# Optimization experiments

Hardware: AMD Instinct MI355X
Metric: run time of the kernel (lower is better)

The kernel has to match this reference:

```python
import jax, jax.numpy as jnp
import numpy as np

N = 8192
IN_F = 256
OUT_F = 64
ALPHA = 0.2
NEG_INF = -9e15


def setup_inputs() -> dict:
    key = jax.random.key(0)
    k1, k2, k3, k4 = jax.random.split(key, 4)
    h = jax.random.normal(k1, (N, IN_F), dtype=jnp.float32)
    W = jax.random.normal(k2, (IN_F, OUT_F), dtype=jnp.float32) * (1.414 / np.sqrt(IN_F))
    a = jax.random.normal(k3, (2 * OUT_F, 1), dtype=jnp.float32) * (1.414 / np.sqrt(2 * OUT_F))
    adj = jax.random.randint(k4, (N, N), 0, 2, dtype=jnp.int32)
    return {"h": h, "W": W, "a": a, "adj": adj}


def reference(h, W, a, adj):
    # Wh: [N, F]
    Wh = h @ W
    # Decompose concat-based attention: e_ij = LeakyReLU(Wh_i . a[:F] + Wh_j . a[F:])
    a1, a2 = a[:OUT_F], a[OUT_F:]
    src = Wh @ a1              # [N, 1] contribution of row i
    dst = Wh @ a2              # [N, 1] contribution of col j
    e = jax.nn.leaky_relu(src + dst.T, negative_slope=ALPHA)  # [N, N]
    e = jnp.where(adj > 0, e, NEG_INF)
    attention = jax.nn.softmax(e, axis=1)
    # dropout is identity in eval mode
    h_prime = attention @ Wh   # [N, F]
    return h_prime
```

## Files before the change

### kernel.cpp

```cpp
#include <hip/hip_runtime.h>

#define NROWS 8192
#define NSPLIT 8
#define JT (NROWS / NSPLIT)
#define NITER (JT / 64)
#define L2E 1.4426950408889634f

typedef __attribute__((ext_vector_type(4))) float f32x4;
typedef __attribute__((ext_vector_type(8))) __bf16 bf16x8;
typedef __attribute__((ext_vector_type(4))) unsigned int u32x4;

__device__ __forceinline__ unsigned short f2bf(float x) {
  unsigned u = __float_as_uint(x);
  u += 0x7fffu + ((u >> 16) & 1u);
  return (unsigned short)(u >> 16);
}

__global__ __launch_bounds__(256) void k_prep(
    const float* __restrict__ h, const float* __restrict__ W,
    const float* __restrict__ a, unsigned short* __restrict__ WhB,
    float* __restrict__ src, float* __restrict__ dst) {
  int i = blockIdx.x * 4 + (threadIdx.x >> 6);
  int lane = threadIdx.x & 63;
  const float* hrow = h + (size_t)i * 256;
  float s = 0.f;
#pragma unroll 4
  for (int k = 0; k < 256; k += 4) {
    float4 hv = *(const float4*)(hrow + k);
    s = fmaf(hv.x, W[(k + 0) * 64 + lane], s);
    s = fmaf(hv.y, W[(k + 1) * 64 + lane], s);
    s = fmaf(hv.z, W[(k + 2) * 64 + lane], s);
    s = fmaf(hv.w, W[(k + 3) * 64 + lane], s);
  }
  int nt = lane >> 4, c = lane & 15;
  int gi = (i >> 3) & 3, e = i & 7;
  int idx = ((((i >> 5) * 4 + nt) * 64) + c + 16 * gi) * 8 + e;
  WhB[idx] = f2bf(s);
  float v1 = s * a[lane];
  float v2 = s * a[64 + lane];
#pragma unroll
  for (int d = 32; d; d >>= 1) {
    v1 += __shfl_xor(v1, d);
    v2 += __shfl_xor(v2, d);
  }
  if (lane == 0) {
    src[i] = v1 * L2E;
    dst[i] = v2 * L2E;
  }
}

__global__ __launch_bounds__(256) void k_dmax(
    const float* __restrict__ dst, float* __restrict__ dmax) {
  __shared__ float red[4];
  float v = -INFINITY;
  for (int i = threadIdx.x; i < NROWS; i += 256) v = fmaxf(v, dst[i]);
#pragma unroll
  for (int d = 32; d; d >>= 1) v = fmaxf(v, __shfl_xor(v, d));
  if ((threadIdx.x & 63) == 0) red[threadIdx.x >> 6] = v;
  __syncthreads();
  if (threadIdx.x == 0)
    *dmax = fmaxf(fmaxf(red[0], red[1]), fmaxf(red[2], red[3]));
}

__global__ __launch_bounds__(256, 4) void k_attn(
    const int* __restrict__ adj, const unsigned short* __restrict__ WhB,
    const float* __restrict__ src, const float* __restrict__ dst,
    const float* __restrict__ dmax,
    float* __restrict__ pl, float* __restrict__ pacc) {
  __shared__ float ldst[JT];
  int task = blockIdx.x * 4 + (threadIdx.x >> 6);
  int sp = task >> 9;
  int mt = task & 511;
  int lane = threadIdx.x & 63;
  int r = lane & 15;
  int g = lane >> 4;
  int row0 = mt * 16;
  int jbase = sp * JT;

  for (int k = threadIdx.x; k < JT; k += 256) ldst[k] = dst[jbase + k];
  __syncthreads();

  unsigned long long mk0 = 0, mk1 = 0, mk2 = 0, mk3 = 0;
  {
    const int* abase = adj + (size_t)row0 * NROWS + jbase + lane;
#pragma unroll
    for (int rr = 0; rr < 16; ++rr) {
      const int* rp = abase + (size_t)rr * NROWS;
#pragma unroll
      for (int ch = 0; ch < 16; ++ch) {
        int v = rp[ch * 64];
        unsigned long long bal = __ballot(v > 0);
        const int holder = ((ch & 3) << 4) + rr;
        if ((ch >> 2) == 0) mk0 = (lane == holder) ? bal : mk0;
        if ((ch >> 2) == 1) mk1 = (lane == holder) ? bal : mk1;
        if ((ch >> 2) == 2) mk2 = (lane == holder) ? bal : mk2;
        if ((ch >> 2) == 3) mk3 = (lane == holder) ? bal : mk3;
      }
    }
  }

  float srcr = src[row0 + r];
  float vB = srcr + *dmax;
  float Mi = fmaxf(vB, 0.2f * vB);

  float lrow = 0.f;
  f32x4 acc[4] = {f32x4{0.f, 0.f, 0.f, 0.f}, f32x4{0.f, 0.f, 0.f, 0.f},
                  f32x4{0.f, 0.f, 0.f, 0.f}, f32x4{0.f, 0.f, 0.f, 0.f}};
  const bf16x8* Bfr = (const bf16x8*)WhB;

#pragma unroll
  for (int it = 0; it < NITER; ++it) {
    const int jb = it * 64;

    unsigned long long pw;
    if ((it >> 2) == 0) pw = __shfl(mk0, ((it & 3) << 4) + r);
    if ((it >> 2) == 1) pw = __shfl(mk1, ((it & 3) << 4) + r);
    if ((it >> 2) == 2) pw = __shfl(mk2, ((it & 3) << 4) + r);
    if ((it >> 2) == 3) pw = __shfl(mk3, ((it & 3) << 4) + r);

    int jc = (jbase + jb) >> 5;
    const bf16x8* bp = Bfr + (size_t)jc * 256 + lane;
    bf16x8 b0 = bp[0];
    bf16x8 b1 = bp[64];
    bf16x8 b2 = bp[128];
    bf16x8 b3 = bp[192];
    bf16x8 b4 = bp[256];
    bf16x8 b5 = bp[320];
    bf16x8 b6 = bp[384];
    bf16x8 b7 = bp[448];

    const float* dl = ldst + jb + 8 * g;
    float4 d0 = *(const float4*)(dl);
    float4 d1 = *(const float4*)(dl + 4);
    float4 d2 = *(const float4*)(dl + 32);
    float4 d3 = *(const float4*)(dl + 36);

    unsigned lo = (unsigned)(pw >> (8 * g));
    unsigned hi = (unsigned)(pw >> (32 + 8 * g));

    float p[16];
#define PE(P, BIT, DD)                    \
  {                                       \
    float v_ = srcr + (DD);               \
    v_ = fmaxf(v_, 0.2f * v_);            \
    float e_ = exp2f(v_ - Mi);            \
    (P) = (BIT) ? e_ : 0.f;               \
  }
    PE(p[0], lo & 1u, d0.x)   PE(p[1], lo & 2u, d0.y)
    PE(p[2], lo & 4u, d0.z)   PE(p[3], lo & 8u, d0.w)
    PE(p[4], lo & 16u, d1.x)  PE(p[5], lo & 32u, d1.y)
    PE(p[6], lo & 64u, d1.z)  PE(p[7], lo & 128u, d1.w)
    PE(p[8], hi & 1u, d2.x)   PE(p[9], hi & 2u, d2.y)
    PE(p[10], hi & 4u, d2.z)  PE(p[11], hi & 8u, d2.w)
    PE(p[12], hi & 16u, d3.x) PE(p[13], hi & 32u, d3.y)
    PE(p[14], hi & 64u, d3.z) PE(p[15], hi & 128u, d3.w)
#undef PE

    unsigned q[8];
#pragma unroll
    for (int t = 0; t < 16; t += 2) {
      lrow += p[t] + p[t + 1];
      unsigned qq;
      asm("v_cvt_pk_bf16_f32 %0, %1, %2" : "=v"(qq) : "v"(p[t]), "v"(p[t + 1]));
      q[t >> 1] = qq;
    }
    u32x4 qv0 = {q[0], q[1], q[2], q[3]};
    u32x4 qv1 = {q[4], q[5], q[6], q[7]};
    bf16x8 A0 = __builtin_bit_cast(bf16x8, qv0);
    bf16x8 A1 = __builtin_bit_cast(bf16x8, qv1);

    __builtin_amdgcn_s_setprio(1);
    acc[0] = __builtin_amdgcn_mfma_f32_16x16x32_bf16(A0, b0, acc[0], 0, 0, 0);
    acc[1] = __builtin_amdgcn_mfma_f32_16x16x32_bf16(A0, b1, acc[1], 0, 0, 0);
    acc[2] = __builtin_amdgcn_mfma_f32_16x16x32_bf16(A0, b2, acc[2], 0, 0, 0);
    acc[3] = __builtin_amdgcn_mfma_f32_16x16x32_bf16(A0, b3, acc[3], 0, 0, 0);
    acc[0] = __builtin_amdgcn_mfma_f32_16x16x32_bf16(A1, b4, acc[0], 0, 0, 0);
    acc[1] = __builtin_amdgcn_mfma_f32_16x16x32_bf16(A1, b5, acc[1], 0, 0, 0);
    acc[2] = __builtin_amdgcn_mfma_f32_16x16x32_bf16(A1, b6, acc[2], 0, 0, 0);
    acc[3] = __builtin_amdgcn_mfma_f32_16x16x32_bf16(A1, b7, acc[3], 0, 0, 0);
    __builtin_amdgcn_s_setprio(0);
  }

  lrow += __shfl_xor(lrow, 16);
  lrow += __shfl_xor(lrow, 32);
  if (lane < 16) pl[sp * NROWS + row0 + lane] = lrow;
#pragma unroll
  for (int nt = 0; nt < 4; nt++)
#pragma unroll
    for (int q2 = 0; q2 < 4; q2++)
      pacc[((size_t)sp * NROWS + row0 + 4 * g + q2) * 64 + nt * 16 + r] = acc[nt][q2];
}

__global__ __launch_bounds__(256) void k_comb(
    const float* __restrict__ pl, const float* __restrict__ pacc,
    float* __restrict__ out) {
  int t = blockIdx.x * 256 + threadIdx.x;
  int row = t >> 6, f = t & 63;
  float L = 0.f, o = 0.f;
#pragma unroll
  for (int s2 = 0; s2 < NSPLIT; s2++) {
    L += pl[s2 * NROWS + row];
    o += pacc[((size_t)s2 * NROWS + row) * 64 + f];
  }
  out[t] = o / L;
}

extern "C" void kernel_launch(void* const* d_in, const int* in_sizes, int n_in,
                              void* d_out, int out_size, void* d_ws, size_t ws_size,
                              hipStream_t stream) {
  const float* h = (const float*)d_in[0];
  const float* W = (const float*)d_in[1];
  const float* a = (const float*)d_in[2];
  const int* adj = (const int*)d_in[3];
  float* out = (float*)d_out;

  char* ws = (char*)d_ws;
  unsigned short* WhB = (unsigned short*)ws;
  float* src = (float*)(ws + 0x100000);
  float* dst = (float*)(ws + 0x108000);
  float* dmax = (float*)(ws + 0x110000);
  float* pl = (float*)(ws + 0x110100);
  float* pacc = (float*)(ws + 0x150100);

  hipLaunchKernelGGL(k_prep, dim3(NROWS / 4), dim3(256), 0, stream, h, W, a, WhB, src, dst);
  hipLaunchKernelGGL(k_dmax, dim3(1), dim3(256), 0, stream, dst, dmax);
  hipLaunchKernelGGL(k_attn, dim3(512 * NSPLIT / 4), dim3(256), 0, stream,
                     adj, WhB, src, dst, dmax, pl, pacc);
  hipLaunchKernelGGL(k_comb, dim3(NROWS * 64 / 256), dim3(256), 0, stream, pl, pacc, out);
}
```

Before: 118.3 us.

## Software-pipeline WhB fragment loads across half-iterations in attention loop

Replaces the fully unrolled attention loop with a non-unrolled loop that splits each 64-column step into two 32-column halves. The B fragments for the next half are loaded while the current half's exp/MFMA work runs, with sched_barriers to hold that order. This aims to hide global load latency with a register-level double buffer. In exchange the full unroll is lost, adding loop overhead and a dynamic mask select, and the last iteration issues one redundant prefetch.

```diff
diff --git a/kernel.cpp b/kernel.cpp
--- a/kernel.cpp
+++ b/kernel.cpp
@@ -103,42 +103,39 @@
   float vB = srcr + *dmax;
   float Mi = fmaxf(vB, 0.2f * vB);
 
-  float lrow = 0.f;
+  float lrA = 0.f, lrB = 0.f;
   f32x4 acc[4] = {f32x4{0.f, 0.f, 0.f, 0.f}, f32x4{0.f, 0.f, 0.f, 0.f},
                   f32x4{0.f, 0.f, 0.f, 0.f}, f32x4{0.f, 0.f, 0.f, 0.f}};
   const bf16x8* Bfr = (const bf16x8*)WhB;
-
-#pragma unroll
-  for (int it = 0; it < NITER; ++it) {
-    const int jb = it * 64;
-
-    unsigned long long pw;
-    if ((it >> 2) == 0) pw = __shfl(mk0, ((it & 3) << 4) + r);
-    if ((it >> 2) == 1) pw = __shfl(mk1, ((it & 3) << 4) + r);
-    if ((it >> 2) == 2) pw = __shfl(mk2, ((it & 3) << 4) + r);
-    if ((it >> 2) == 3) pw = __shfl(mk3, ((it & 3) << 4) + r);
-
-    int jc = (jbase + jb) >> 5;
-    const bf16x8* bp = Bfr + (size_t)jc * 256 + lane;
-    bf16x8 b0 = bp[0];
-    bf16x8 b1 = bp[64];
-    bf16x8 b2 = bp[128];
-    bf16x8 b3 = bp[192];
-    bf16x8 b4 = bp[256];
-    bf16x8 b5 = bp[320];
-    bf16x8 b6 = bp[384];
-    bf16x8 b7 = bp[448];
-
-    const float* dl = ldst + jb + 8 * g;
-    float4 d0 = *(const float4*)(dl);
-    float4 d1 = *(const float4*)(dl + 4);
-    float4 d2 = *(const float4*)(dl + 32);
-    float4 d3 = *(const float4*)(dl + 36);
-
-    unsigned lo = (unsigned)(pw >> (8 * g));
-    unsigned hi = (unsigned)(pw >> (32 + 8 * g));
-
-    float p[16];
+  const int jc0 = jbase >> 5;
+
+#define HALF(B0, B1, B2, B3, BITS, DOFF)                                   \
+  {                                                                        \
+    const float4* dlp = (const float4*)(ldst + (DOFF));                    \
+    float4 dA = dlp[0];                                                    \
+    float4 dB = dlp[1];                                                    \
+    unsigned bt_ = (BITS);                                                 \
+    float p0, p1, p2, p3, p4, p5, p6, p7;                                  \
+    PE(p0, bt_ & 1u, dA.x)   PE(p1, bt_ & 2u, dA.y)                        \
+    PE(p2, bt_ & 4u, dA.z)   PE(p3, bt_ & 8u, dA.w)                        \
+    PE(p4, bt_ & 16u, dB.x)  PE(p5, bt_ & 32u, dB.y)                       \
+    PE(p6, bt_ & 64u, dB.z)  PE(p7, bt_ & 128u, dB.w)                      \
+    lrA += (p0 + p1) + (p2 + p3);                                          \
+    lrB += (p4 + p5) + (p6 + p7);                                          \
+    unsigned q0, q1, q2, q3;                                               \
+    asm("v_cvt_pk_bf16_f32 %0, %1, %2" : "=v"(q0) : "v"(p0), "v"(p1));     \
+    asm("v_cvt_pk_bf16_f32 %0, %1, %2" : "=v"(q1) : "v"(p2), "v"(p3));     \
+    asm("v_cvt_pk_bf16_f32 %0, %1, %2" : "=v"(q2) : "v"(p4), "v"(p5));     \
+    asm("v_cvt_pk_bf16_f32 %0, %1, %2" : "=v"(q3) : "v"(p6), "v"(p7));     \
+    u32x4 qv = {q0, q1, q2, q3};                                           \
+    bf16x8 Af = __builtin_bit_cast(bf16x8, qv);                            \
+    __builtin_amdgcn_s_setprio(1);                                         \
+    acc[0] = __builtin_amdgcn_mfma_f32_16x16x32_bf16(Af, B0, acc[0], 0, 0, 0); \
+    acc[1] = __builtin_amdgcn_mfma_f32_16x16x32_bf16(Af, B1, acc[1], 0, 0, 0); \
+    acc[2] = __builtin_amdgcn_mfma_f32_16x16x32_bf16(Af, B2, acc[2], 0, 0, 0); \
+    acc[3] = __builtin_amdgcn_mfma_f32_16x16x32_bf16(Af, B3, acc[3], 0, 0, 0); \
+    __builtin_amdgcn_s_setprio(0);                                         \
+  }
 #define PE(P, BIT, DD)                    \
   {                                       \
     float v_ = srcr + (DD);               \
@@ -146,41 +143,35 @@
     float e_ = exp2f(v_ - Mi);            \
     (P) = (BIT) ? e_ : 0.f;               \
   }
-    PE(p[0], lo & 1u, d0.x)   PE(p[1], lo & 2u, d0.y)
-    PE(p[2], lo & 4u, d0.z)   PE(p[3], lo & 8u, d0.w)
-    PE(p[4], lo & 16u, d1.x)  PE(p[5], lo & 32u, d1.y)
-    PE(p[6], lo & 64u, d1.z)  PE(p[7], lo & 128u, d1.w)
-    PE(p[8], hi & 1u, d2.x)   PE(p[9], hi & 2u, d2.y)
-    PE(p[10], hi & 4u, d2.z)  PE(p[11], hi & 8u, d2.w)
-    PE(p[12], hi & 16u, d3.x) PE(p[13], hi & 32u, d3.y)
-    PE(p[14], hi & 64u, d3.z) PE(p[15], hi & 128u, d3.w)
+
+  const bf16x8* bpA = Bfr + (size_t)jc0 * 256 + lane;
+  bf16x8 a0 = bpA[0], a1 = bpA[64], a2 = bpA[128], a3 = bpA[192];
+
+#pragma unroll 1
+  for (int it = 0; it < NITER; ++it) {
+    int sel = it >> 2;
+    unsigned long long msrc = (sel == 0) ? mk0
+                            : (sel == 1) ? mk1
+                            : (sel == 2) ? mk2 : mk3;
+    unsigned long long pw = __shfl(msrc, ((it & 3) << 4) + r);
+
+    const bf16x8* bpB = Bfr + (size_t)(jc0 + 2 * it + 1) * 256 + lane;
+    bf16x8 c0 = bpB[0], c1 = bpB[64], c2 = bpB[128], c3 = bpB[192];
+    __builtin_amdgcn_sched_barrier(0);
+
+    HALF(a0, a1, a2, a3, (unsigned)(pw >> (8 * g)), it * 64 + 8 * g)
+
+    int jn = (it == NITER - 1) ? jc0 : jc0 + 2 * it + 2;
+    const bf16x8* bpN = Bfr + (size_t)jn * 256 + lane;
+    a0 = bpN[0]; a1 = bpN[64]; a2 = bpN[128]; a3 = bpN[192];
+    __builtin_amdgcn_sched_barrier(0);
+
+    HALF(c0, c1, c2, c3, (unsigned)(pw >> (32 + 8 * g)), it * 64 + 32 + 8 * g)
+  }
 #undef PE
-
-    unsigned q[8];
-#pragma unroll
-    for (int t = 0; t < 16; t += 2) {
-      lrow += p[t] + p[t + 1];
-      unsigned qq;
-      asm("v_cvt_pk_bf16_f32 %0, %1, %2" : "=v"(qq) : "v"(p[t]), "v"(p[t + 1]));
-      q[t >> 1] = qq;
-    }
-    u32x4 qv0 = {q[0], q[1], q[2], q[3]};
-    u32x4 qv1 = {q[4], q[5], q[6], q[7]};
-    bf16x8 A0 = __builtin_bit_cast(bf16x8, qv0);
-    bf16x8 A1 = __builtin_bit_cast(bf16x8, qv1);
-
-    __builtin_amdgcn_s_setprio(1);
-    acc[0] = __builtin_amdgcn_mfma_f32_16x16x32_bf16(A0, b0, acc[0], 0, 0, 0);
-    acc[1] = __builtin_amdgcn_mfma_f32_16x16x32_bf16(A0, b1, acc[1], 0, 0, 0);
-    acc[2] = __builtin_amdgcn_mfma_f32_16x16x32_bf16(A0, b2, acc[2], 0, 0, 0);
-    acc[3] = __builtin_amdgcn_mfma_f32_16x16x32_bf16(A0, b3, acc[3], 0, 0, 0);
-    acc[0] = __builtin_amdgcn_mfma_f32_16x16x32_bf16(A1, b4, acc[0], 0, 0, 0);
-    acc[1] = __builtin_amdgcn_mfma_f32_16x16x32_bf16(A1, b5, acc[1], 0, 0, 0);
-    acc[2] = __builtin_amdgcn_mfma_f32_16x16x32_bf16(A1, b6, acc[2], 0, 0, 0);
-    acc[3] = __builtin_amdgcn_mfma_f32_16x16x32_bf16(A1, b7, acc[3], 0, 0, 0);
-    __builtin_amdgcn_s_setprio(0);
-  }
-
+#undef HALF
+
+  float lrow = lrA + lrB;
   lrow += __shfl_xor(lrow, 16);
   lrow += __shfl_xor(lrow, 32);
   if (lane < 16) pl[sp * NROWS + row0 + lane] = lrow;
```

Result: no change. 118.8 us (+0.4%).

## Give each wave 32 rows so WhB fragments feed two row tiles, and split columns 16 ways

Applied to the files above, without the earlier changes.

Each wave now processes two 16-row tiles (32 rows) over a 512-column slice, with the column split doubled to 16. Every loaded WhB bf16 fragment then feeds two MFMAs instead of one, halving B-operand global traffic per unit of work. The main loop is no longer unrolled. The cost is more accumulator registers, twice as many partial results for the combine kernel to read, and a larger pacc workspace offset.

```diff
diff --git a/kernel.cpp b/kernel.cpp
--- a/kernel.cpp
+++ b/kernel.cpp
@@ -1,7 +1,7 @@
 #include <hip/hip_runtime.h>
 
 #define NROWS 8192
-#define NSPLIT 8
+#define NSPLIT 16
 #define JT (NROWS / NSPLIT)
 #define NITER (JT / 64)
 #define L2E 1.4426950408889634f
@@ -69,12 +69,12 @@
     float* __restrict__ pl, float* __restrict__ pacc) {
   __shared__ float ldst[JT];
   int task = blockIdx.x * 4 + (threadIdx.x >> 6);
-  int sp = task >> 9;
-  int mt = task & 511;
+  int sp = task >> 8;
+  int pt = task & 255;
   int lane = threadIdx.x & 63;
   int r = lane & 15;
   int g = lane >> 4;
-  int row0 = mt * 16;
+  int row0p = pt * 32;
   int jbase = sp * JT;
 
   for (int k = threadIdx.x; k < JT; k += 256) ldst[k] = dst[jbase + k];
@@ -82,43 +82,56 @@
 
   unsigned long long mk0 = 0, mk1 = 0, mk2 = 0, mk3 = 0;
   {
-    const int* abase = adj + (size_t)row0 * NROWS + jbase + lane;
-#pragma unroll
-    for (int rr = 0; rr < 16; ++rr) {
+    const int* abase = adj + (size_t)row0p * NROWS + jbase + lane;
+#pragma unroll
+    for (int rr = 0; rr < 32; ++rr) {
       const int* rp = abase + (size_t)rr * NROWS;
 #pragma unroll
-      for (int ch = 0; ch < 16; ++ch) {
+      for (int ch = 0; ch < 8; ++ch) {
         int v = rp[ch * 64];
         unsigned long long bal = __ballot(v > 0);
-        const int holder = ((ch & 3) << 4) + rr;
-        if ((ch >> 2) == 0) mk0 = (lane == holder) ? bal : mk0;
-        if ((ch >> 2) == 1) mk1 = (lane == holder) ? bal : mk1;
-        if ((ch >> 2) == 2) mk2 = (lane == holder) ? bal : mk2;
-        if ((ch >> 2) == 3) mk3 = (lane == holder) ? bal : mk3;
+        const int holder = ((ch & 1) << 5) + rr;
+        if ((ch >> 1) == 0) mk0 = (lane == holder) ? bal : mk0;
+        if ((ch >> 1) == 1) mk1 = (lane == holder) ? bal : mk1;
+        if ((ch >> 1) == 2) mk2 = (lane == holder) ? bal : mk2;
+        if ((ch >> 1) == 3) mk3 = (lane == holder) ? bal : mk3;
       }
     }
   }
 
-  float srcr = src[row0 + r];
-  float vB = srcr + *dmax;
-  float Mi = fmaxf(vB, 0.2f * vB);
-
-  float lrow = 0.f;
-  f32x4 acc[4] = {f32x4{0.f, 0.f, 0.f, 0.f}, f32x4{0.f, 0.f, 0.f, 0.f},
-                  f32x4{0.f, 0.f, 0.f, 0.f}, f32x4{0.f, 0.f, 0.f, 0.f}};
+  float dmv = *dmax;
+  float srcA = src[row0p + r];
+  float srcB = src[row0p + 16 + r];
+  float vA = srcA + dmv, vBv = srcB + dmv;
+  float MiA = fmaxf(vA, 0.2f * vA);
+  float MiB = fmaxf(vBv, 0.2f * vBv);
+
+  float lrA = 0.f, lrB = 0.f;
+  f32x4 accA[4] = {f32x4{0.f, 0.f, 0.f, 0.f}, f32x4{0.f, 0.f, 0.f, 0.f},
+                   f32x4{0.f, 0.f, 0.f, 0.f}, f32x4{0.f, 0.f, 0.f, 0.f}};
+  f32x4 accB[4] = {f32x4{0.f, 0.f, 0.f, 0.f}, f32x4{0.f, 0.f, 0.f, 0.f},
+                   f32x4{0.f, 0.f, 0.f, 0.f}, f32x4{0.f, 0.f, 0.f, 0.f}};
   const bf16x8* Bfr = (const bf16x8*)WhB;
 
-#pragma unroll
+#define PE(P, BIT, DD, SRC, MI)           \
+  {                                       \
+    float v_ = (SRC) + (DD);              \
+    v_ = fmaxf(v_, 0.2f * v_);            \
+    float e_ = exp2f(v_ - (MI));          \
+    (P) = (BIT) ? e_ : 0.f;               \
+  }
+
+#pragma unroll 1
   for (int it = 0; it < NITER; ++it) {
-    const int jb = it * 64;
-
-    unsigned long long pw;
-    if ((it >> 2) == 0) pw = __shfl(mk0, ((it & 3) << 4) + r);
-    if ((it >> 2) == 1) pw = __shfl(mk1, ((it & 3) << 4) + r);
-    if ((it >> 2) == 2) pw = __shfl(mk2, ((it & 3) << 4) + r);
-    if ((it >> 2) == 3) pw = __shfl(mk3, ((it & 3) << 4) + r);
-
-    int jc = (jbase + jb) >> 5;
+    int sel = it >> 1;
+    unsigned long long msrc = (sel == 0) ? mk0
+                            : (sel == 1) ? mk1
+                            : (sel == 2) ? mk2 : mk3;
+    int lsub = (it & 1) << 5;
+    unsigned long long pwA = __shfl(msrc, lsub + r);
+    unsigned long long pwB = __shfl(msrc, lsub + 16 + r);
+
+    int jc = sp * 16 + 2 * it;
     const bf16x8* bp = Bfr + (size_t)jc * 256 + lane;
     bf16x8 b0 = bp[0];
     bf16x8 b1 = bp[64];
@@ -129,66 +142,102 @@
     bf16x8 b6 = bp[384];
     bf16x8 b7 = bp[448];
 
-    const float* dl = ldst + jb + 8 * g;
+    const float* dl = ldst + it * 64 + 8 * g;
     float4 d0 = *(const float4*)(dl);
     float4 d1 = *(const float4*)(dl + 4);
     float4 d2 = *(const float4*)(dl + 32);
     float4 d3 = *(const float4*)(dl + 36);
 
-    unsigned lo = (unsigned)(pw >> (8 * g));
-    unsigned hi = (unsigned)(pw >> (32 + 8 * g));
-
-    float p[16];
-#define PE(P, BIT, DD)                    \
-  {                                       \
-    float v_ = srcr + (DD);               \
-    v_ = fmaxf(v_, 0.2f * v_);            \
-    float e_ = exp2f(v_ - Mi);            \
-    (P) = (BIT) ? e_ : 0.f;               \
-  }
-    PE(p[0], lo & 1u, d0.x)   PE(p[1], lo & 2u, d0.y)
-    PE(p[2], lo & 4u, d0.z)   PE(p[3], lo & 8u, d0.w)
-    PE(p[4], lo & 16u, d1.x)  PE(p[5], lo & 32u, d1.y)
-    PE(p[6], lo & 64u, d1.z)  PE(p[7], lo & 128u, d1.w)
-    PE(p[8], hi & 1u, d2.x)   PE(p[9], hi & 2u, d2.y)
-    PE(p[10], hi & 4u, d2.z)  PE(p[11], hi & 8u, d2.w)
-    PE(p[12], hi & 16u, d3.x) PE(p[13], hi & 32u, d3.y)
-    PE(p[14], hi & 64u, d3.z) PE(p[15], hi & 128u, d3.w)
+    unsigned loA = (unsigned)(pwA >> (8 * g)), hiA = (unsigned)(pwA >> (32 + 8 * g));
+    unsigned loB = (unsigned)(pwB >> (8 * g)), hiB = (unsigned)(pwB >> (32 + 8 * g));
+
+    float p0, p1, p2, p3, p4, p5, p6, p7;
+    PE(p0, loA & 1u, d0.x, srcA, MiA)   PE(p1, loA & 2u, d0.y, srcA, MiA)
+    PE(p2, loA & 4u, d0.z, srcA, MiA)   PE(p3, loA & 8u, d0.w, srcA, MiA)
+    PE(p4, loA & 16u, d1.x, srcA, MiA)  PE(p5, loA & 32u, d1.y, srcA, MiA)
+    PE(p6, loA & 64u, d1.z, srcA, MiA)  PE(p7, loA & 128u, d1.w, srcA, MiA)
+    lrA += ((p0 + p1) + (p2 + p3)) + ((p4 + p5) + (p6 + p7));
+    unsigned qa0, qa1, qa2, qa3;
+    asm("v_cvt_pk_bf16_f32 %0, %1, %2" : "=v"(qa0) : "v"(p0), "v"(p1));
+    asm("v_cvt_pk_bf16_f32 %0, %1, %2" : "=v"(qa1) : "v"(p2), "v"(p3));
+    asm("v_cvt_pk_bf16_f32 %0, %1, %2" : "=v"(qa2) : "v"(p4), "v"(p5));
+    asm("v_cvt_pk_bf16_f32 %0, %1, %2" : "=v"(qa3) : "v"(p6), "v"(p7));
+    PE(p0, hiA & 1u, d2.x, srcA, MiA)   PE(p1, hiA & 2u, d2.y, srcA, MiA)
+    PE(p2, hiA & 4u, d2.z, srcA, MiA)   PE(p3, hiA & 8u, d2.w, srcA, MiA)
+    PE(p4, hiA & 16u, d3.x, srcA, MiA)  PE(p5, hiA & 32u, d3.y, srcA, MiA)
+    PE(p6, hiA & 64u, d3.z, srcA, MiA)  PE(p7, hiA & 128u, d3.w, srcA, MiA)
+    lrA += ((p0 + p1) + (p2 + p3)) + ((p4 + p5) + (p6 + p7));
+    unsigned qa4, qa5, qa6, qa7;
+    asm("v_cvt_pk_bf16_f32 %0, %1, %2" : "=v"(qa4) : "v"(p0), "v"(p1));
+    asm("v_cvt_pk_bf16_f32 %0, %1, %2" : "=v"(qa5) : "v"(p2), "v"(p3));
+    asm("v_cvt_pk_bf16_f32 %0, %1, %2" : "=v"(qa6) : "v"(p4), "v"(p5));
+    asm("v_cvt_pk_bf16_f32 %0, %1, %2" : "=v"(qa7) : "v"(p6), "v"(p7));
+    u32x4 qvA0 = {qa0, qa1, qa2, qa3};
+    u32x4 qvA1 = {qa4, qa5, qa6, qa7};
+    bf16x8 A0 = __builtin_bit_cast(bf16x8, qvA0);
+    bf16x8 A1 = __builtin_bit_cast(bf16x8, qvA1);
+
+    PE(p0, loB & 1u, d0.x, srcB, MiB)   PE(p1, loB & 2u, d0.y, srcB, MiB)
+    PE(p2, loB & 4u, d0.z, srcB, MiB)   PE(p3, loB & 8u, d0.w, srcB, MiB)
+    PE(p4, loB & 16u, d1.x, srcB, MiB)  PE(p5, loB & 32u, d1.y, srcB, MiB)
+    PE(p6, loB & 64u, d1.z, srcB, MiB)  PE(p7, loB & 128u, d1.w, srcB, MiB)
+    lrB += ((p0 + p1) + (p2 + p3)) + ((p4 + p5) + (p6 + p7));
+    unsigned qb0, qb1, qb2, qb3;
+    asm("v_cvt_pk_bf16_f32 %0, %1, %2" : "=v"(qb0) : "v"(p0), "v"(p1));
+    asm("v_cvt_pk_bf16_f32 %0, %1, %2" : "=v"(qb1) : "v"(p2), "v"(p3));
+    asm("v_cvt_pk_bf16_f32 %0, %1, %2" : "=v"(qb2) : "v"(p4), "v"(p5));
+    asm("v_cvt_pk_bf16_f32 %0, %1, %2" : "=v"(qb3) : "v"(p6), "v"(p7));
+    PE(p0, hiB & 1u, d2.x, srcB, MiB)   PE(p1, hiB & 2u, d2.y, srcB, MiB)
+    PE(p2, hiB & 4u, d2.z, srcB, MiB)   PE(p3, hiB & 8u, d2.w, srcB, MiB)
+    PE(p4, hiB & 16u, d3.x, srcB, MiB)  PE(p5, hiB & 32u, d3.y, srcB, MiB)
+    PE(p6, hiB & 64u, d3.z, srcB, MiB)  PE(p7, hiB & 128u, d3.w, srcB, MiB)
+    lrB += ((p0 + p1) + (p2 + p3)) + ((p4 + p5) + (p6 + p7));
+    unsigned qb4, qb5, qb6, qb7;
+    asm("v_cvt_pk_bf16_f32 %0, %1, %2" : "=v"(qb4) : "v"(p0), "v"(p1));
+    asm("v_cvt_pk_bf16_f32 %0, %1, %2" : "=v"(qb5) : "v"(p2), "v"(p3));
+    asm("v_cvt_pk_bf16_f32 %0, %1, %2" : "=v"(qb6) : "v"(p4), "v"(p5));
+    asm("v_cvt_pk_bf16_f32 %0, %1, %2" : "=v"(qb7) : "v"(p6), "v"(p7));
+    u32x4 qvB0 = {qb0, qb1, qb2, qb3};
+    u32x4 qvB1 = {qb4, qb5, qb6, qb7};
+    bf16x8 A0b = __builtin_bit_cast(bf16x8, qvB0);
+    bf16x8 A1b = __builtin_bit_cast(bf16x8, qvB1);
+
+    __builtin_amdgcn_s_setprio(1);
+    accA[0] = __builtin_amdgcn_mfma_f32_16x16x32_bf16(A0, b0, accA[0], 0, 0, 0);
+    accB[0] = __builtin_amdgcn_mfma_f32_16x16x32_bf16(A0b, b0, accB[0], 0, 0, 0);
+    accA[1] = __builtin_amdgcn_mfma_f32_16x16x32_bf16(A0, b1, accA[1], 0, 0, 0);
+    accB[1] = __builtin_amdgcn_mfma_f32_16x16x32_bf16(A0b, b1, accB[1], 0, 0, 0);
+    accA[2] = __builtin_amdgcn_mfma_f32_16x16x32_bf16(A0, b2, accA[2], 0, 0, 0);
+    accB[2] = __builtin_amdgcn_mfma_f32_16x16x32_bf16(A0b, b2, accB[2], 0, 0, 0);
+    accA[3] = __builtin_amdgcn_mfma_f32_16x16x32_bf16(A0, b3, accA[3], 0, 0, 0);
+    accB[3] = __builtin_amdgcn_mfma_f32_16x16x32_bf16(A0b, b3, accB[3], 0, 0, 0);
+    accA[0] = __builtin_amdgcn_mfma_f32_16x16x32_bf16(A1, b4, accA[0], 0, 0, 0);
+    accB[0] = __builtin_amdgcn_mfma_f32_16x16x32_bf16(A1b, b4, accB[0], 0, 0, 0);
+    accA[1] = __builtin_amdgcn_mfma_f32_16x16x32_bf16(A1, b5, accA[1], 0, 0, 0);
+    accB[1] = __builtin_amdgcn_mfma_f32_16x16x32_bf16(A1b, b5, accB[1], 0, 0, 0);
+    accA[2] = __builtin_amdgcn_mfma_f32_16x16x32_bf16(A1, b6, accA[2], 0, 0, 0);
+    accB[2] = __builtin_amdgcn_mfma_f32_16x16x32_bf16(A1b, b6, accB[2], 0, 0, 0);
+    accA[3] = __builtin_amdgcn_mfma_f32_16x16x32_bf16(A1, b7, accA[3], 0, 0, 0);
+    accB[3] = __builtin_amdgcn_mfma_f32_16x16x32_bf16(A1b, b7, accB[3], 0, 0, 0);
+    __builtin_amdgcn_s_setprio(0);
+  }
 #undef PE
 
-    unsigned q[8];
-#pragma unroll
-    for (int t = 0; t < 16; t += 2) {
-      lrow += p[t] + p[t + 1];
-      unsigned qq;
-      asm("v_cvt_pk_bf16_f32 %0, %1, %2" : "=v"(qq) : "v"(p[t]), "v"(p[t + 1]));
-      q[t >> 1] = qq;
+  lrA += __shfl_xor(lrA, 16);
+  lrA += __shfl_xor(lrA, 32);
+  lrB += __shfl_xor(lrB, 16);
+  lrB += __shfl_xor(lrB, 32);
+  if (lane < 16) {
+    pl[sp * NROWS + row0p + lane] = lrA;
+    pl[sp * NROWS + row0p + 16 + lane] = lrB;
+  }
+#pragma unroll
+  for (int nt = 0; nt < 4; nt++)
+#pragma unroll
+    for (int q2 = 0; q2 < 4; q2++) {
+      pacc[((size_t)sp * NROWS + row0p + 4 * g + q2) * 64 + nt * 16 + r] = accA[nt][q2];
+      pacc[((size_t)sp * NROWS + row0p + 16 + 4 * g + q2) * 64 + nt * 16 + r] = accB[nt][q2];
     }
-    u32x4 qv0 = {q[0], q[1], q[2], q[3]};
-    u32x4 qv1 = {q[4], q[5], q[6], q[7]};
-    bf16x8 A0 = __builtin_bit_cast(bf16x8, qv0);
-    bf16x8 A1 = __builtin_bit_cast(bf16x8, qv1);
-
-    __builtin_amdgcn_s_setprio(1);
-    acc[0] = __builtin_amdgcn_mfma_f32_16x16x32_bf16(A0, b0, acc[0], 0, 0, 0);
-    acc[1] = __builtin_amdgcn_mfma_f32_16x16x32_bf16(A0, b1, acc[1], 0, 0, 0);
-    acc[2] = __builtin_amdgcn_mfma_f32_16x16x32_bf16(A0, b2, acc[2], 0, 0, 0);
-    acc[3] = __builtin_amdgcn_mfma_f32_16x16x32_bf16(A0, b3, acc[3], 0, 0, 0);
-    acc[0] = __builtin_amdgcn_mfma_f32_16x16x32_bf16(A1, b4, acc[0], 0, 0, 0);
-    acc[1] = __builtin_amdgcn_mfma_f32_16x16x32_bf16(A1, b5, acc[1], 0, 0, 0);
-    acc[2] = __builtin_amdgcn_mfma_f32_16x16x32_bf16(A1, b6, acc[2], 0, 0, 0);
-    acc[3] = __builtin_amdgcn_mfma_f32_16x16x32_bf16(A1, b7, acc[3], 0, 0, 0);
-    __builtin_amdgcn_s_setprio(0);
-  }
-
-  lrow += __shfl_xor(lrow, 16);
-  lrow += __shfl_xor(lrow, 32);
-  if (lane < 16) pl[sp * NROWS + row0 + lane] = lrow;
-#pragma unroll
-  for (int nt = 0; nt < 4; nt++)
-#pragma unroll
-    for (int q2 = 0; q2 < 4; q2++)
-      pacc[((size_t)sp * NROWS + row0 + 4 * g + q2) * 64 + nt * 16 + r] = acc[nt][q2];
 }
 
 __global__ __launch_bounds__(256) void k_comb(
@@ -220,11 +269,11 @@
   float* dst = (float*)(ws + 0x108000);
   float* dmax = (float*)(ws + 0x110000);
   float* pl = (float*)(ws + 0x110100);
-  float* pacc = (float*)(ws + 0x150100);
+  float* pacc = (float*)(ws + 0x190100);
 
   hipLaunchKernelGGL(k_prep, dim3(NROWS / 4), dim3(256), 0, stream, h, W, a, WhB, src, dst);
   hipLaunchKernelGGL(k_dmax, dim3(1), dim3(256), 0, stream, dst, dmax);
-  hipLaunchKernelGGL(k_attn, dim3(512 * NSPLIT / 4), dim3(256), 0, stream,
+  hipLaunchKernelGGL(k_attn, dim3(1024), dim3(256), 0, stream,
                      adj, WhB, src, dst, dmax, pl, pacc);
   hipLaunchKernelGGL(k_comb, dim3(NROWS * 64 / 256), dim3(256), 0, stream, pl, pacc, out);
 }
```

Result: slower. 157.2 us (+32.9%).
